# Optimization experiments

Hardware: AMD Instinct MI355X
Metric: run time of the kernel (lower is better)

## Reference

```python
import math
import jax, jax.numpy as jnp
import numpy as np

NUM_BINS = 128
NUM_FREQS = 64
HEAD_DIM = 2 * NUM_FREQS
NUM_QUERIES = 16384
EPS = 1e-8


def setup_inputs() -> dict:
    key = jax.random.key(0)
    k1, k2 = jax.random.split(key, 2)
    Q = jax.random.normal(k1, (NUM_QUERIES, HEAD_DIM), dtype=jnp.float32)
    rotated_probes = jax.random.normal(k2, (NUM_BINS, HEAD_DIM), dtype=jnp.float32)
    # probes are expected pre-normalized
    rotated_probes = rotated_probes / (jnp.linalg.norm(rotated_probes, axis=-1, keepdims=True) + EPS)
    init_value = math.log(math.e - 1.0)  # softplus(init)=1
    q_weights_raw = jnp.full((NUM_BINS, NUM_FREQS), init_value, dtype=jnp.float32)
    q_magnitude_weights = jnp.zeros((NUM_BINS, NUM_FREQS), dtype=jnp.float32)
    q_bias = jnp.zeros((NUM_BINS,), dtype=jnp.float32)
    return {
        "Q": Q,
        "rotated_probes": rotated_probes,
        "q_weights_raw": q_weights_raw,
        "q_magnitude_weights": q_magnitude_weights,
        "q_bias": q_bias,
    }


def reference(Q, rotated_probes, q_weights_raw, q_magnitude_weights, q_bias):
    F = NUM_FREQS
    # L2 normalize Q
    norm = jnp.linalg.norm(Q, axis=-1, keepdims=True)
    Qn = Q / (norm + EPS)
    Q_real, Q_imag = Qn[:, :F], Qn[:, F:]            # (Nq, F)
    P_real, P_imag = rotated_probes[:, :F], rotated_probes[:, F:]  # (B, F)
    # broadcast per-frequency complex error and distance: (Nq, B, F)
    err_r = P_real[None, :, :] - Q_real[:, None, :]
    err_i = P_imag[None, :, :] - Q_imag[:, None, :]
    distance = jnp.sqrt(err_r * err_r + err_i * err_i + EPS)
    # magnitude features on normalized Q: (Nq, F)
    Q_mag = jnp.sqrt(Q_real * Q_real + Q_imag * Q_imag + EPS)
    eff_w = -jax.nn.softplus(q_weights_raw)          # (B, F), negative weights
    distance_term = jnp.einsum('qbf,bf->qb', distance, eff_w)
    magnitude_term = Q_mag @ q_magnitude_weights.T   # (Nq, B)
    return distance_term + magnitude_term + q_bias[None, :]
```

## Files before the change

kernel.cpp:

```cpp
#include <hip/hip_runtime.h>

#define NBINS 128
#define NFREQ 64
#define HDIM 128
#define NQ 16384
#define EPSF 1e-8f

typedef _Float16 h2 __attribute__((ext_vector_type(2)));
#define B2(x) __builtin_bit_cast(h2, (x))
#define U32(x) __builtin_bit_cast(unsigned, (x))

__device__ __forceinline__ h2 cvt_pk(float a, float b) {
  return __builtin_bit_cast(h2, __builtin_amdgcn_cvt_pkrtz(a, b));
}

#define WS_NEEDED (64 * 1024)

__global__ __launch_bounds__(256) void pack8(
    const float* __restrict__ probes,
    const float* __restrict__ wraw,
    const float* __restrict__ mw,
    unsigned* __restrict__ ws) {
  const int id = blockIdx.x * 256 + threadIdx.x;
  if (id >= 1024) return;
  const int c = id >> 7, b = id & 127;
  const float* pb = probes + b * HDIM + c * 8;
  const float* wb = wraw + b * NFREQ + c * 8;
  const float* mb = mw + b * NFREQ + c * 8;
  float pr[8], pi[8], w[8], m[8];
  *reinterpret_cast<float4*>(&pr[0]) = *reinterpret_cast<const float4*>(pb);
  *reinterpret_cast<float4*>(&pr[4]) = *reinterpret_cast<const float4*>(pb + 4);
  *reinterpret_cast<float4*>(&pi[0]) = *reinterpret_cast<const float4*>(pb + NFREQ);
  *reinterpret_cast<float4*>(&pi[4]) = *reinterpret_cast<const float4*>(pb + NFREQ + 4);
  *reinterpret_cast<float4*>(&w[0])  = *reinterpret_cast<const float4*>(wb);
  *reinterpret_cast<float4*>(&w[4])  = *reinterpret_cast<const float4*>(wb + 4);
  *reinterpret_cast<float4*>(&m[0])  = *reinterpret_cast<const float4*>(mb);
  *reinterpret_cast<float4*>(&m[4])  = *reinterpret_cast<const float4*>(mb + 4);
  unsigned ep[8], wp[4], mp[4];
  #pragma unroll
  for (int j = 0; j < 8; ++j) {
    h2 v = {(_Float16)pr[j], (_Float16)pi[j]};
    ep[j] = U32(v);
  }
  #pragma unroll
  for (int k = 0; k < 4; ++k) {
    float w0 = w[2 * k], w1 = w[2 * k + 1];
    float n0 = -(fmaxf(w0, 0.0f) + log1pf(expf(-fabsf(w0))));
    float n1 = -(fmaxf(w1, 0.0f) + log1pf(expf(-fabsf(w1))));
    h2 vw = {(_Float16)n0, (_Float16)n1};
    h2 vm = {(_Float16)m[2 * k], (_Float16)m[2 * k + 1]};
    wp[k] = U32(vw);
    mp[k] = U32(vm);
  }
  unsigned* EP = ws + (size_t)(c * 128 + b) * 8;
  *reinterpret_cast<uint4*>(EP)     = make_uint4(ep[0], ep[1], ep[2], ep[3]);
  *reinterpret_cast<uint4*>(EP + 4) = make_uint4(ep[4], ep[5], ep[6], ep[7]);
  unsigned* WP = ws + 8192 + (size_t)(c * 128 + b) * 4;
  *reinterpret_cast<uint4*>(WP) = make_uint4(wp[0], wp[1], wp[2], wp[3]);
  unsigned* MP = ws + 12288 + (size_t)(c * 128 + b) * 4;
  *reinterpret_cast<uint4*>(MP) = make_uint4(mp[0], mp[1], mp[2], mp[3]);
}

__global__ __launch_bounds__(256) void scorer8(
    const float* __restrict__ Q,
    const unsigned* __restrict__ ws,
    const float* __restrict__ bias,
    float* __restrict__ out) {
  __shared__ __align__(16) unsigned qep[16 * 64];
  __shared__ __align__(16) unsigned qqm[16 * 32];
  const int t = threadIdx.x;
  const int qblk = blockIdx.x * 16;

  {
    const int q = t >> 4;
    const int sub = t & 15;
    const float* qp = Q + (size_t)(qblk + q) * HDIM;
    const float4 re = *reinterpret_cast<const float4*>(qp + sub * 4);
    const float4 im = *reinterpret_cast<const float4*>(qp + NFREQ + sub * 4);
    float s = re.x * re.x + re.y * re.y + re.z * re.z + re.w * re.w
            + im.x * im.x + im.y * im.y + im.z * im.z + im.w * im.w;
    s += __shfl_xor(s, 1, 16);
    s += __shfl_xor(s, 2, 16);
    s += __shfl_xor(s, 4, 16);
    s += __shfl_xor(s, 8, 16);
    const float inv = 1.0f / (__builtin_amdgcn_sqrtf(s) + EPSF);
    const float qr[4] = {re.x * inv, re.y * inv, re.z * inv, re.w * inv};
    const float qi[4] = {im.x * inv, im.y * inv, im.z * inv, im.w * inv};
    unsigned ew[4], mwd[2];
    float qm[4];
    #pragma unroll
    for (int k = 0; k < 4; ++k) {
      h2 v = {(_Float16)(-qr[k]), (_Float16)(-qi[k])};
      ew[k] = U32(v);
      qm[k] = __builtin_amdgcn_sqrtf(fmaf(qr[k], qr[k], fmaf(qi[k], qi[k], EPSF)));
    }
    {
      h2 v0 = {(_Float16)qm[0], (_Float16)qm[1]};
      h2 v1 = {(_Float16)qm[2], (_Float16)qm[3]};
      mwd[0] = U32(v0);
      mwd[1] = U32(v1);
    }
    *reinterpret_cast<uint4*>(&qep[q * 64 + sub * 4]) =
        make_uint4(ew[0], ew[1], ew[2], ew[3]);
    *reinterpret_cast<uint2*>(&qqm[q * 32 + sub * 2]) = make_uint2(mwd[0], mwd[1]);
  }
  __syncthreads();

  const int lane = t & 63;
  const int w = __builtin_amdgcn_readfirstlane(t >> 6);
  const int q0 = w * 4;
  const unsigned* EP = ws;
  const unsigned* WP = ws + 8192;
  const unsigned* MP = ws + 12288;

  float dacc[4][2], macc[4][2];
  #pragma unroll
  for (int q = 0; q < 4; ++q) {
    dacc[q][0] = dacc[q][1] = 0.0f;
    macc[q][0] = macc[q][1] = 0.0f;
  }

  #pragma unroll 1
  for (int c = 0; c < 8; ++c) {
    const uint4 e0a = *reinterpret_cast<const uint4*>(EP + (size_t)(c * 128 + lane) * 8);
    const uint4 e0b = *reinterpret_cast<const uint4*>(EP + (size_t)(c * 128 + lane) * 8 + 4);
    const uint4 e1a = *reinterpret_cast<const uint4*>(EP + (size_t)(c * 128 + 64 + lane) * 8);
    const uint4 e1b = *reinterpret_cast<const uint4*>(EP + (size_t)(c * 128 + 64 + lane) * 8 + 4);
    const uint4 w0v = *reinterpret_cast<const uint4*>(WP + (size_t)(c * 128 + lane) * 4);
    const uint4 w1v = *reinterpret_cast<const uint4*>(WP + (size_t)(c * 128 + 64 + lane) * 4);
    const uint4 m0v = *reinterpret_cast<const uint4*>(MP + (size_t)(c * 128 + lane) * 4);
    const uint4 m1v = *reinterpret_cast<const uint4*>(MP + (size_t)(c * 128 + 64 + lane) * 4);
    const unsigned ep[2][8] = {
        {e0a.x, e0a.y, e0a.z, e0a.w, e0b.x, e0b.y, e0b.z, e0b.w},
        {e1a.x, e1a.y, e1a.z, e1a.w, e1b.x, e1b.y, e1b.z, e1b.w}};
    const unsigned wp[2][4] = {{w0v.x, w0v.y, w0v.z, w0v.w},
                               {w1v.x, w1v.y, w1v.z, w1v.w}};
    const unsigned mp[2][4] = {{m0v.x, m0v.y, m0v.z, m0v.w},
                               {m1v.x, m1v.y, m1v.z, m1v.w}};
    #pragma unroll
    for (int q = 0; q < 4; ++q) {
      const uint4 qa = *reinterpret_cast<const uint4*>(&qep[(q0 + q) * 64 + c * 8]);
      const uint4 qb = *reinterpret_cast<const uint4*>(&qep[(q0 + q) * 64 + c * 8 + 4]);
      const uint4 qm4 = *reinterpret_cast<const uint4*>(&qqm[(q0 + q) * 32 + c * 4]);
      const unsigned qe[8] = {qa.x, qa.y, qa.z, qa.w, qb.x, qb.y, qb.z, qb.w};
      const unsigned qmw[4] = {qm4.x, qm4.y, qm4.z, qm4.w};
      #pragma unroll
      for (int bc = 0; bc < 2; ++bc) {
        float da = dacc[q][bc], ma = macc[q][bc];
        #pragma unroll
        for (int fp = 0; fp < 4; ++fp) {
          h2 e0 = B2(ep[bc][2 * fp]) + B2(qe[2 * fp]);
          h2 e1 = B2(ep[bc][2 * fp + 1]) + B2(qe[2 * fp + 1]);
          float d0 = __builtin_amdgcn_fdot2(e0, e0, EPSF, false);
          float d1 = __builtin_amdgcn_fdot2(e1, e1, EPSF, false);
          h2 dp = cvt_pk(__builtin_amdgcn_sqrtf(d0), __builtin_amdgcn_sqrtf(d1));
          da = __builtin_amdgcn_fdot2(dp, B2(wp[bc][fp]), da, false);
          ma = __builtin_amdgcn_fdot2(B2(qmw[fp]), B2(mp[bc][fp]), ma, false);
        }
        dacc[q][bc] = da;
        macc[q][bc] = ma;
      }
    }
  }

  const float bias0 = bias[lane];
  const float bias1 = bias[64 + lane];
  #pragma unroll
  for (int q = 0; q < 4; ++q) {
    const size_t row = (size_t)(qblk + q0 + q) * NBINS;
    out[row + lane]      = dacc[q][0] + macc[q][0] + bias0;
    out[row + 64 + lane] = dacc[q][1] + macc[q][1] + bias1;
  }
}

extern "C" void kernel_launch(void* const* d_in, const int* in_sizes, int n_in,
                              void* d_out, int out_size, void* d_ws, size_t ws_size,
                              hipStream_t stream) {
  const float* Q      = (const float*)d_in[0];
  const float* probes = (const float*)d_in[1];
  const float* wraw   = (const float*)d_in[2];
  const float* mw     = (const float*)d_in[3];
  const float* bias   = (const float*)d_in[4];
  float* out = (float*)d_out;
  unsigned* ws = (unsigned*)d_ws;

  pack8<<<4, 256, 0, stream>>>(probes, wraw, mw, ws);
  scorer8<<<NQ / 16, 256, 0, stream>>>(Q, ws, bias, out);
}
```

Baseline: 38.16 us.

## Split frequency chunks across two waves with LDS reduction, smaller blocks

The scorer now uses 128-thread blocks handling 4 queries each. The two waves split the 8 frequency chunks between them instead of splitting queries, and their partial sums are combined through shared memory before the store. The distance and magnitude accumulators are merged into one. This is meant to raise the number of blocks and occupancy and to halve the per-wave probe loads per query group. The cost is an extra barrier, an LDS reduction, and four times as many blocks each reloading the probe tables.

```diff
diff --git a/kernel.cpp b/kernel.cpp
--- a/kernel.cpp
+++ b/kernel.cpp
@@ -61,75 +61,63 @@
   *reinterpret_cast<uint4*>(MP) = make_uint4(mp[0], mp[1], mp[2], mp[3]);
 }
 
-__global__ __launch_bounds__(256) void scorer8(
+__global__ __launch_bounds__(128, 8) void scorer11(
     const float* __restrict__ Q,
     const unsigned* __restrict__ ws,
     const float* __restrict__ bias,
     float* __restrict__ out) {
-  __shared__ __align__(16) unsigned qep[16 * 64];
-  __shared__ __align__(16) unsigned qqm[16 * 32];
+  __shared__ __align__(16) unsigned qep[4 * 64];
+  __shared__ __align__(16) unsigned qqm[4 * 32];
+  __shared__ float part[4][2][64];
   const int t = threadIdx.x;
-  const int qblk = blockIdx.x * 16;
+  const int qblk = blockIdx.x * 4;
 
   {
-    const int q = t >> 4;
-    const int sub = t & 15;
-    const float* qp = Q + (size_t)(qblk + q) * HDIM;
-    const float4 re = *reinterpret_cast<const float4*>(qp + sub * 4);
-    const float4 im = *reinterpret_cast<const float4*>(qp + NFREQ + sub * 4);
-    float s = re.x * re.x + re.y * re.y + re.z * re.z + re.w * re.w
-            + im.x * im.x + im.y * im.y + im.z * im.z + im.w * im.w;
-    s += __shfl_xor(s, 1, 16);
-    s += __shfl_xor(s, 2, 16);
-    s += __shfl_xor(s, 4, 16);
-    s += __shfl_xor(s, 8, 16);
+    const int q = t >> 5;
+    const int seg = t & 31;
+    const float* qp = Q + (size_t)(qblk + q) * HDIM + seg * 2;
+    const float2 r = *reinterpret_cast<const float2*>(qp);
+    const float2 i = *reinterpret_cast<const float2*>(qp + NFREQ);
+    float s = r.x * r.x + r.y * r.y + i.x * i.x + i.y * i.y;
+    s += __shfl_xor(s, 1, 32);
+    s += __shfl_xor(s, 2, 32);
+    s += __shfl_xor(s, 4, 32);
+    s += __shfl_xor(s, 8, 32);
+    s += __shfl_xor(s, 16, 32);
     const float inv = 1.0f / (__builtin_amdgcn_sqrtf(s) + EPSF);
-    const float qr[4] = {re.x * inv, re.y * inv, re.z * inv, re.w * inv};
-    const float qi[4] = {im.x * inv, im.y * inv, im.z * inv, im.w * inv};
-    unsigned ew[4], mwd[2];
-    float qm[4];
-    #pragma unroll
-    for (int k = 0; k < 4; ++k) {
-      h2 v = {(_Float16)(-qr[k]), (_Float16)(-qi[k])};
-      ew[k] = U32(v);
-      qm[k] = __builtin_amdgcn_sqrtf(fmaf(qr[k], qr[k], fmaf(qi[k], qi[k], EPSF)));
-    }
-    {
-      h2 v0 = {(_Float16)qm[0], (_Float16)qm[1]};
-      h2 v1 = {(_Float16)qm[2], (_Float16)qm[3]};
-      mwd[0] = U32(v0);
-      mwd[1] = U32(v1);
-    }
-    *reinterpret_cast<uint4*>(&qep[q * 64 + sub * 4]) =
-        make_uint4(ew[0], ew[1], ew[2], ew[3]);
-    *reinterpret_cast<uint2*>(&qqm[q * 32 + sub * 2]) = make_uint2(mwd[0], mwd[1]);
+    const float qr0 = r.x * inv, qi0 = i.x * inv;
+    const float qr1 = r.y * inv, qi1 = i.y * inv;
+    h2 e0 = {(_Float16)(-qr0), (_Float16)(-qi0)};
+    h2 e1 = {(_Float16)(-qr1), (_Float16)(-qi1)};
+    *reinterpret_cast<uint2*>(&qep[q * 64 + seg * 2]) = make_uint2(U32(e0), U32(e1));
+    const float qm0 = __builtin_amdgcn_sqrtf(fmaf(qr0, qr0, fmaf(qi0, qi0, EPSF)));
+    const float qm1 = __builtin_amdgcn_sqrtf(fmaf(qr1, qr1, fmaf(qi1, qi1, EPSF)));
+    h2 vm = {(_Float16)qm0, (_Float16)qm1};
+    qqm[q * 32 + seg] = U32(vm);
   }
   __syncthreads();
 
   const int lane = t & 63;
-  const int w = __builtin_amdgcn_readfirstlane(t >> 6);
-  const int q0 = w * 4;
-  const unsigned* EP = ws;
-  const unsigned* WP = ws + 8192;
-  const unsigned* MP = ws + 12288;
+  const int fh = __builtin_amdgcn_readfirstlane(t >> 6);
 
-  float dacc[4][2], macc[4][2];
+  float acc[4][2];
   #pragma unroll
-  for (int q = 0; q < 4; ++q) {
-    dacc[q][0] = dacc[q][1] = 0.0f;
-    macc[q][0] = macc[q][1] = 0.0f;
-  }
+  for (int q = 0; q < 4; ++q) acc[q][0] = acc[q][1] = 0.0f;
 
   #pragma unroll 1
-  for (int c = 0; c < 8; ++c) {
-    const uint4 e0a = *reinterpret_cast<const uint4*>(EP + (size_t)(c * 128 + lane) * 8);
-    const uint4 e0b = *reinterpret_cast<const uint4*>(EP + (size_t)(c * 128 + lane) * 8 + 4);
-    const uint4 e1a = *reinterpret_cast<const uint4*>(EP + (size_t)(c * 128 + 64 + lane) * 8);
-    const uint4 e1b = *reinterpret_cast<const uint4*>(EP + (size_t)(c * 128 + 64 + lane) * 8 + 4);
-    const uint4 w0v = *reinterpret_cast<const uint4*>(WP + (size_t)(c * 128 + lane) * 4);
-    const uint4 w1v = *reinterpret_cast<const uint4*>(WP + (size_t)(c * 128 + 64 + lane) * 4);
-    const uint4 m0v = *reinterpret_cast<const uint4*>(MP + (size_t)(c * 128 + lane) * 4);
-    const uint4 m1v = *reinterpret_cast<const uint4*>(MP + (size_t)(c * 128 + 64 + lane) * 4);
+  for (int ci = 0; ci < 4; ++ci) {
+    const int c = fh * 4 + ci;
+    const unsigned* EPb = ws + (size_t)(c * 128 + lane) * 8;
+    const unsigned* WPb = ws + 8192 + (size_t)(c * 128 + lane) * 4;
+    const unsigned* MPb = ws + 12288 + (size_t)(c * 128 + lane) * 4;
+    const uint4 e0a = *reinterpret_cast<const uint4*>(EPb);
+    const uint4 e0b = *reinterpret_cast<const uint4*>(EPb + 4);
+    const uint4 e1a = *reinterpret_cast<const uint4*>(EPb + 512);
+    const uint4 e1b = *reinterpret_cast<const uint4*>(EPb + 516);
+    const uint4 w0v = *reinterpret_cast<const uint4*>(WPb);
+    const uint4 w1v = *reinterpret_cast<const uint4*>(WPb + 256);
+    const uint4 m0v = *reinterpret_cast<const uint4*>(MPb);
+    const uint4 m1v = *reinterpret_cast<const uint4*>(MPb + 256);
     const unsigned ep[2][8] = {
         {e0a.x, e0a.y, e0a.z, e0a.w, e0b.x, e0b.y, e0b.z, e0b.w},
         {e1a.x, e1a.y, e1a.z, e1a.w, e1b.x, e1b.y, e1b.z, e1b.w}};
@@ -139,37 +127,46 @@
                                {m1v.x, m1v.y, m1v.z, m1v.w}};
     #pragma unroll
     for (int q = 0; q < 4; ++q) {
-      const uint4 qa = *reinterpret_cast<const uint4*>(&qep[(q0 + q) * 64 + c * 8]);
-      const uint4 qb = *reinterpret_cast<const uint4*>(&qep[(q0 + q) * 64 + c * 8 + 4]);
-      const uint4 qm4 = *reinterpret_cast<const uint4*>(&qqm[(q0 + q) * 32 + c * 4]);
+      const uint4 qa = *reinterpret_cast<const uint4*>(&qep[q * 64 + c * 8]);
+      const uint4 qb = *reinterpret_cast<const uint4*>(&qep[q * 64 + c * 8 + 4]);
+      const uint4 qm4 = *reinterpret_cast<const uint4*>(&qqm[q * 32 + c * 4]);
       const unsigned qe[8] = {qa.x, qa.y, qa.z, qa.w, qb.x, qb.y, qb.z, qb.w};
       const unsigned qmw[4] = {qm4.x, qm4.y, qm4.z, qm4.w};
       #pragma unroll
       for (int bc = 0; bc < 2; ++bc) {
-        float da = dacc[q][bc], ma = macc[q][bc];
+        float da = acc[q][bc];
         #pragma unroll
         for (int fp = 0; fp < 4; ++fp) {
-          h2 e0 = B2(ep[bc][2 * fp]) + B2(qe[2 * fp]);
+          h2 e0 = B2(ep[bc][2 * fp])     + B2(qe[2 * fp]);
           h2 e1 = B2(ep[bc][2 * fp + 1]) + B2(qe[2 * fp + 1]);
           float d0 = __builtin_amdgcn_fdot2(e0, e0, EPSF, false);
           float d1 = __builtin_amdgcn_fdot2(e1, e1, EPSF, false);
           h2 dp = cvt_pk(__builtin_amdgcn_sqrtf(d0), __builtin_amdgcn_sqrtf(d1));
           da = __builtin_amdgcn_fdot2(dp, B2(wp[bc][fp]), da, false);
-          ma = __builtin_amdgcn_fdot2(B2(qmw[fp]), B2(mp[bc][fp]), ma, false);
+          da = __builtin_amdgcn_fdot2(B2(qmw[fp]), B2(mp[bc][fp]), da, false);
         }
-        dacc[q][bc] = da;
-        macc[q][bc] = ma;
+        acc[q][bc] = da;
       }
     }
   }
 
-  const float bias0 = bias[lane];
-  const float bias1 = bias[64 + lane];
-  #pragma unroll
-  for (int q = 0; q < 4; ++q) {
-    const size_t row = (size_t)(qblk + q0 + q) * NBINS;
-    out[row + lane]      = dacc[q][0] + macc[q][0] + bias0;
-    out[row + 64 + lane] = dacc[q][1] + macc[q][1] + bias1;
+  if (fh == 1) {
+    #pragma unroll
+    for (int q = 0; q < 4; ++q) {
+      part[q][0][lane] = acc[q][0];
+      part[q][1][lane] = acc[q][1];
+    }
+  }
+  __syncthreads();
+  if (fh == 0) {
+    const float bias0 = bias[lane];
+    const float bias1 = bias[64 + lane];
+    #pragma unroll
+    for (int q = 0; q < 4; ++q) {
+      const size_t row = (size_t)(qblk + q) * NBINS;
+      out[row + lane]      = acc[q][0] + part[q][0][lane] + bias0;
+      out[row + 64 + lane] = acc[q][1] + part[q][1][lane] + bias1;
+    }
   }
 }
 
@@ -185,5 +182,5 @@
   unsigned* ws = (unsigned*)d_ws;
 
   pack8<<<4, 256, 0, stream>>>(probes, wraw, mw, ws);
-  scorer8<<<NQ / 16, 256, 0, stream>>>(Q, ws, bias, out);
+  scorer11<<<NQ / 4, 128, 0, stream>>>(Q, ws, bias, out);
 }
```

New measurement: 37.32 us. 1.02x faster.
